# Kernel tuning notes

Hardware: AMD Instinct MI355X
Metric: run time of the kernel (lower is better)

The kernel has to match this reference:

```python
import jax, jax.numpy as jnp
import numpy as np
import math

T, NE, DA = 4096, 2048, 2048
LAYER_ID, NUM_LAYERS = 12, 24


def setup_inputs() -> dict:
    key = jax.random.key(0)
    kx, kk, kv, kr, ko = jax.random.split(key, 5)
    # --- learned params, initialised exactly like the haiku module ---
    ratio_0_to_1 = LAYER_ID / (NUM_LAYERS - 1)
    ratio_1_to_almost0 = 1.0 - LAYER_ID / NUM_LAYERS
    time_first = jnp.ones(DA, jnp.float32) * math.log(0.3) + \
        jnp.array([(i + 1) % 3 - 1 for i in range(DA)], jnp.float32) * 0.5
    time_decay = -5 + 8 * (jnp.arange(DA, dtype=jnp.float32) / (DA - 1)) ** (0.7 + 1.3 * ratio_0_to_1)
    ddd = jnp.arange(DA, dtype=jnp.float32)[jnp.newaxis, :] / DA  # [1, DA]
    time_mix_k = jnp.power(ddd, ratio_1_to_almost0)
    time_mix_v = time_mix_k + 0.3 * ratio_0_to_1
    time_mix_r = jnp.power(ddd, ratio_1_to_almost0 * 0.5)
    s = 1.0 / math.sqrt(NE)
    return {
        'x': jax.random.normal(kx, (T, NE), jnp.float32),
        'time_first': time_first,
        'time_decay': time_decay,
        'time_mix_k': time_mix_k,
        'time_mix_v': time_mix_v,
        'time_mix_r': time_mix_r,
        'W_key': jax.random.normal(kk, (NE, DA), jnp.float32) * s,
        'W_value': jax.random.normal(kv, (NE, DA), jnp.float32) * s,
        'W_receptance': jax.random.normal(kr, (NE, DA), jnp.float32) * s,
        'W_output': jax.random.normal(ko, (DA, NE), jnp.float32) * (1.0 / math.sqrt(DA)),
    }


def _wkv(time_decay, time_first, k, v):
    # k, v: [T, C]. Vectorized over channels; sequential scan over time.
    dtype = k.dtype
    w = -jnp.exp(time_decay.astype(jnp.float32))  # [C]
    u = time_first.astype(jnp.float32)            # [C]
    kf = k.astype(jnp.float32)
    vf = v.astype(jnp.float32)
    C = kf.shape[1]

    def body(carry, kv):
        p, q, o = carry
        kt, vt = kv
        # output at t (includes bonus u on current token)
        no = jnp.maximum(o, u + kt)
        A = jnp.exp(o - no)
        B = jnp.exp(u + kt - no)
        y = (A * p + B * vt) / (A * q + B)
        # state update (decay w applied to running sums)
        no2 = jnp.maximum(w + o, kt)
        A2 = jnp.exp(w + o - no2)
        B2 = jnp.exp(kt - no2)
        return (A2 * p + B2 * vt, A2 * q + B2, no2), y

    init = (jnp.zeros(C, jnp.float32), jnp.zeros(C, jnp.float32),
            jnp.full(C, -1e38, jnp.float32))
    _, ys = jax.lax.scan(body, init, (kf, vf))  # ys: [T, C]
    return ys.astype(dtype)


def reference(x, time_first, time_decay, time_mix_k, time_mix_v, time_mix_r,
              W_key, W_value, W_receptance, W_output):
    # time shift: shift sequence right by one (zero-pad first position)
    xx = jnp.pad(x, [(1, 0), (0, 0)])[:-1, :]
    xk = x * time_mix_k + xx * (1 - time_mix_k)
    xv = x * time_mix_v + xx * (1 - time_mix_v)
    xr = x * time_mix_r + xx * (1 - time_mix_r)
    k = xk @ W_key          # [T, DA]
    v = xv @ W_value        # [T, DA]
    r = xr @ W_receptance   # [T, DA]
    sr = jax.nn.sigmoid(r)
    wkv = _wkv(time_decay, time_first, k, v)  # [T, DA]
    return (sr * wkv) @ W_output              # [T, NE]
```

## Files before the change

kernel.cpp:

```cpp
#include <hip/hip_runtime.h>
#include <math.h>

#define T_ 4096
#define NE_ 2048
#define DA_ 2048
#define TDA ((size_t)T_ * NE_)

constexpr int NC = 64;
constexpr int CL = T_ / NC;

typedef __attribute__((ext_vector_type(8))) short short8;
typedef __attribute__((ext_vector_type(4))) float f32x4;

__device__ __forceinline__ unsigned short f2bf(float f) {
  union { float f; unsigned int u; } v; v.f = f;
  unsigned int u = v.u;
  return (unsigned short)((u + 0x7FFFu + ((u >> 16) & 1u)) >> 16);
}
__device__ __forceinline__ float bf2f(unsigned short h) {
  union { unsigned int u; float f; } v; v.u = ((unsigned int)h) << 16;
  return v.f;
}

__device__ __forceinline__ void gload_lds16(const void* g, void* l) {
  __builtin_amdgcn_global_load_lds(
      (const __attribute__((address_space(1))) void*)g,
      (__attribute__((address_space(3))) void*)l, 16, 0, 0);
}

__device__ __forceinline__ void gemm_core(
    const unsigned short* __restrict__ A, const unsigned short* __restrict__ Bt,
    void* __restrict__ C, int c_bf16)
{
  constexpr int K = 2048, N = 2048;
  __shared__ unsigned short As[128 * 32];
  __shared__ unsigned short Bs[128 * 32];

  const int tid = threadIdx.x;
  const int w = tid >> 6, lane = tid & 63;
  const int bm = blockIdx.x * 128, bn = blockIdx.y * 128;
  const int wr = w >> 1, wc = w & 1;

  f32x4 acc[4][4];
#pragma unroll
  for (int m = 0; m < 4; ++m)
#pragma unroll
    for (int n = 0; n < 4; ++n) acc[m][n] = (f32x4){0.f, 0.f, 0.f, 0.f};

  const int sr = lane >> 2;
  const int gc = (lane & 3) ^ ((lane >> 3) & 3);
  const size_t gA0 = (size_t)(bm + w * 32 + sr) * K + gc * 8;
  const size_t gB0 = (size_t)(bn + w * 32 + sr) * K + gc * 8;
  unsigned short* lA = &As[w * 1024];
  unsigned short* lB = &Bs[w * 1024];

  const int lr = lane & 15, ck = lane >> 4;
  const int coff = ((ck ^ ((lr >> 1) & 3)) << 3);
  const int arow = wr * 64 + lr;
  const int brow = wc * 64 + lr;

  for (int kk = 0; kk < K; kk += 32) {
    __syncthreads();
    gload_lds16(A + gA0 + kk, lA);
    gload_lds16(A + gA0 + kk + (size_t)16 * K, lA + 512);
    gload_lds16(Bt + gB0 + kk, lB);
    gload_lds16(Bt + gB0 + kk + (size_t)16 * K, lB + 512);
    __syncthreads();

    short8 af[4], bfr[4];
#pragma unroll
    for (int m = 0; m < 4; ++m)
      af[m] = *reinterpret_cast<const short8*>(&As[(arow + m * 16) * 32 + coff]);
#pragma unroll
    for (int n = 0; n < 4; ++n)
      bfr[n] = *reinterpret_cast<const short8*>(&Bs[(brow + n * 16) * 32 + coff]);
#pragma unroll
    for (int m = 0; m < 4; ++m)
#pragma unroll
      for (int n = 0; n < 4; ++n)
        acc[m][n] = __builtin_amdgcn_mfma_f32_16x16x32_bf16(af[m], bfr[n], acc[m][n], 0, 0, 0);
  }

  const int crow0 = bm + wr * 64 + (lane >> 4) * 4;
  const int ccol0 = bn + wc * 64 + (lane & 15);
  if (c_bf16) {
    unsigned short* Cb = (unsigned short*)C;
#pragma unroll
    for (int m = 0; m < 4; ++m)
#pragma unroll
      for (int n = 0; n < 4; ++n)
#pragma unroll
        for (int j = 0; j < 4; ++j)
          Cb[(size_t)(crow0 + m * 16 + j) * N + ccol0 + n * 16] = f2bf(acc[m][n][j]);
  } else {
    float* Cf = (float*)C;
#pragma unroll
    for (int m = 0; m < 4; ++m)
#pragma unroll
      for (int n = 0; n < 4; ++n)
#pragma unroll
        for (int j = 0; j < 4; ++j)
          Cf[(size_t)(crow0 + m * 16 + j) * N + ccol0 + n * 16] = acc[m][n][j];
  }
}

__global__ __launch_bounds__(256) void gemm3_bf16(
    const unsigned short* __restrict__ A0, const unsigned short* __restrict__ A1,
    const unsigned short* __restrict__ A2,
    const unsigned short* __restrict__ B0, const unsigned short* __restrict__ B1,
    const unsigned short* __restrict__ B2,
    void* __restrict__ C0, void* __restrict__ C1, void* __restrict__ C2,
    int c_bf16)
{
  const int z = blockIdx.z;
  const unsigned short* A = (z == 0) ? A0 : (z == 1) ? A1 : A2;
  const unsigned short* B = (z == 0) ? B0 : (z == 1) ? B1 : B2;
  void* C = (z == 0) ? C0 : (z == 1) ? C1 : C2;
  gemm_core(A, B, C, c_bf16);
}

__global__ __launch_bounds__(256) void transpose_cvt3(
    const float* __restrict__ W0, const float* __restrict__ W1,
    const float* __restrict__ W2,
    unsigned short* __restrict__ O0, unsigned short* __restrict__ O1,
    unsigned short* __restrict__ O2)
{
  constexpr int K = 2048, N = 2048;
  const int z = blockIdx.z;
  const float* W = (z == 0) ? W0 : (z == 1) ? W1 : W2;
  unsigned short* O = (z == 0) ? O0 : (z == 1) ? O1 : O2;

  __shared__ float tile[32][33];
  const int bk = blockIdx.y * 32;
  const int bn = blockIdx.x * 32;
  const int tx = threadIdx.x;
  const int ty = threadIdx.y;
#pragma unroll
  for (int i = 0; i < 32; i += 8)
    tile[ty + i][tx] = W[(size_t)(bk + ty + i) * N + bn + tx];
  __syncthreads();
#pragma unroll
  for (int i = 0; i < 32; i += 8)
    O[(size_t)(bn + ty + i) * K + bk + tx] = f2bf(tile[tx][ty + i]);
}

__global__ __launch_bounds__(256) void mix3_cvt(
    const float* __restrict__ x,
    const float* __restrict__ tmk, const float* __restrict__ tmv,
    const float* __restrict__ tmr,
    unsigned short* __restrict__ ok, unsigned short* __restrict__ ov,
    unsigned short* __restrict__ orr)
{
  const int i = blockIdx.x * 256 + threadIdx.x;
  const int t = i / (NE_ / 4);
  const int e4 = i % (NE_ / 4);
  const float4 xc = reinterpret_cast<const float4*>(x)[i];
  float4 xp = make_float4(0.f, 0.f, 0.f, 0.f);
  if (t > 0) xp = reinterpret_cast<const float4*>(x)[i - NE_ / 4];
  const float4 dx = make_float4(xc.x - xp.x, xc.y - xp.y, xc.z - xp.z, xc.w - xp.w);

  float4 m;
  ushort4 r;
  m = reinterpret_cast<const float4*>(tmk)[e4];
  r.x = f2bf(xp.x + m.x * dx.x); r.y = f2bf(xp.y + m.y * dx.y);
  r.z = f2bf(xp.z + m.z * dx.z); r.w = f2bf(xp.w + m.w * dx.w);
  reinterpret_cast<ushort4*>(ok)[i] = r;
  m = reinterpret_cast<const float4*>(tmv)[e4];
  r.x = f2bf(xp.x + m.x * dx.x); r.y = f2bf(xp.y + m.y * dx.y);
  r.z = f2bf(xp.z + m.z * dx.z); r.w = f2bf(xp.w + m.w * dx.w);
  reinterpret_cast<ushort4*>(ov)[i] = r;
  m = reinterpret_cast<const float4*>(tmr)[e4];
  r.x = f2bf(xp.x + m.x * dx.x); r.y = f2bf(xp.y + m.y * dx.y);
  r.z = f2bf(xp.z + m.z * dx.z); r.w = f2bf(xp.w + m.w * dx.w);
  reinterpret_cast<ushort4*>(orr)[i] = r;
}

__global__ __launch_bounds__(256) void wkv_pass1(
    const unsigned short* __restrict__ Kb, const unsigned short* __restrict__ Vb,
    const float* __restrict__ td, float* __restrict__ SP, float* __restrict__ SQ)
{
  const int c4 = blockIdx.x * 256 + threadIdx.x;
  const int chunk = blockIdx.y;
  const int t0 = chunk * CL;
  const float4 tdv = reinterpret_cast<const float4*>(td)[c4];
  float lam[4] = {__expf(-__expf(tdv.x)), __expf(-__expf(tdv.y)),
                  __expf(-__expf(tdv.z)), __expf(-__expf(tdv.w))};
  float P[4] = {0.f, 0.f, 0.f, 0.f}, Q[4] = {0.f, 0.f, 0.f, 0.f};
  for (int t = t0; t < t0 + CL; ++t) {
    const ushort4 kq = reinterpret_cast<const ushort4*>(Kb + (size_t)t * DA_)[c4];
    const ushort4 vq = reinterpret_cast<const ushort4*>(Vb + (size_t)t * DA_)[c4];
    const float kf[4] = {bf2f(kq.x), bf2f(kq.y), bf2f(kq.z), bf2f(kq.w)};
    const float vf[4] = {bf2f(vq.x), bf2f(vq.y), bf2f(vq.z), bf2f(vq.w)};
#pragma unroll
    for (int j = 0; j < 4; ++j) {
      const float e = __expf(kf[j]);
      P[j] = fmaf(lam[j], P[j], e * vf[j]);
      Q[j] = fmaf(lam[j], Q[j], e);
    }
  }
  reinterpret_cast<float4*>(SP + (size_t)chunk * DA_)[c4] = (float4){P[0], P[1], P[2], P[3]};
  reinterpret_cast<float4*>(SQ + (size_t)chunk * DA_)[c4] = (float4){Q[0], Q[1], Q[2], Q[3]};
}

__global__ __launch_bounds__(256) void wkv_pass2(
    const float* __restrict__ td, float* __restrict__ SP, float* __restrict__ SQ)
{
  const int c4 = blockIdx.x * 256 + threadIdx.x;
  const float4 tdv = reinterpret_cast<const float4*>(td)[c4];
  float lamL[4] = {__expf(-__expf(tdv.x) * (float)CL), __expf(-__expf(tdv.y) * (float)CL),
                   __expf(-__expf(tdv.z) * (float)CL), __expf(-__expf(tdv.w) * (float)CL)};
  float P[4] = {0.f, 0.f, 0.f, 0.f}, Q[4] = {0.f, 0.f, 0.f, 0.f};
  for (int i = 0; i < NC; ++i) {
    float4* sp4 = reinterpret_cast<float4*>(SP + (size_t)i * DA_) + c4;
    float4* sq4 = reinterpret_cast<float4*>(SQ + (size_t)i * DA_) + c4;
    const float4 sp = *sp4, sq = *sq4;
    *sp4 = (float4){P[0], P[1], P[2], P[3]};
    *sq4 = (float4){Q[0], Q[1], Q[2], Q[3]};
    P[0] = fmaf(lamL[0], P[0], sp.x); Q[0] = fmaf(lamL[0], Q[0], sq.x);
    P[1] = fmaf(lamL[1], P[1], sp.y); Q[1] = fmaf(lamL[1], Q[1], sq.y);
    P[2] = fmaf(lamL[2], P[2], sp.z); Q[2] = fmaf(lamL[2], Q[2], sq.z);
    P[3] = fmaf(lamL[3], P[3], sp.w); Q[3] = fmaf(lamL[3], Q[3], sq.w);
  }
}

__global__ __launch_bounds__(256) void wkv_pass3(
    const unsigned short* __restrict__ Kb, const unsigned short* __restrict__ Vb,
    const unsigned short* __restrict__ Rb, unsigned short* __restrict__ Ab,
    const float* __restrict__ td, const float* __restrict__ tf,
    const float* __restrict__ SP, const float* __restrict__ SQ)
{
  const int c4 = blockIdx.x * 256 + threadIdx.x;
  const int chunk = blockIdx.y;
  const int t0 = chunk * CL;
  const float4 tdv = reinterpret_cast<const float4*>(td)[c4];
  const float4 tfv = reinterpret_cast<const float4*>(tf)[c4];
  const float lam[4] = {__expf(-__expf(tdv.x)), __expf(-__expf(tdv.y)),
                        __expf(-__expf(tdv.z)), __expf(-__expf(tdv.w))};
  const float eu[4] = {__expf(tfv.x), __expf(tfv.y), __expf(tfv.z), __expf(tfv.w)};
  const float4 p0 = reinterpret_cast<const float4*>(SP + (size_t)chunk * DA_)[c4];
  const float4 q0 = reinterpret_cast<const float4*>(SQ + (size_t)chunk * DA_)[c4];
  float P[4] = {p0.x, p0.y, p0.z, p0.w};
  float Q[4] = {q0.x, q0.y, q0.z, q0.w};
  for (int t = t0; t < t0 + CL; ++t) {
    const ushort4 kq = reinterpret_cast<const ushort4*>(Kb + (size_t)t * DA_)[c4];
    const ushort4 vq = reinterpret_cast<const ushort4*>(Vb + (size_t)t * DA_)[c4];
    const ushort4 rq = reinterpret_cast<const ushort4*>(Rb + (size_t)t * DA_)[c4];
    const float kf[4] = {bf2f(kq.x), bf2f(kq.y), bf2f(kq.z), bf2f(kq.w)};
    const float vf[4] = {bf2f(vq.x), bf2f(vq.y), bf2f(vq.z), bf2f(vq.w)};
    const float rf[4] = {bf2f(rq.x), bf2f(rq.y), bf2f(rq.z), bf2f(rq.w)};
    ushort4 a;
    unsigned short* ap = (unsigned short*)&a;
#pragma unroll
    for (int j = 0; j < 4; ++j) {
      const float e = __expf(kf[j]);
      const float b = eu[j] * e;
      const float y = (P[j] + b * vf[j]) / (Q[j] + b);
      const float sr = 1.f / (1.f + __expf(-rf[j]));
      ap[j] = f2bf(sr * y);
      P[j] = fmaf(lam[j], P[j], e * vf[j]);
      Q[j] = fmaf(lam[j], Q[j], e);
    }
    reinterpret_cast<ushort4*>(Ab + (size_t)t * DA_)[c4] = a;
  }
}

extern "C" void kernel_launch(void* const* d_in, const int* in_sizes, int n_in,
                              void* d_out, int out_size, void* d_ws, size_t ws_size,
                              hipStream_t stream)
{
  const float* x   = (const float*)d_in[0];
  const float* tf  = (const float*)d_in[1];
  const float* td  = (const float*)d_in[2];
  const float* tmk = (const float*)d_in[3];
  const float* tmv = (const float*)d_in[4];
  const float* tmr = (const float*)d_in[5];
  const float* Wk  = (const float*)d_in[6];
  const float* Wv  = (const float*)d_in[7];
  const float* Wr  = (const float*)d_in[8];
  const float* Wo  = (const float*)d_in[9];
  float* out = (float*)d_out;

  const size_t MB = 1024 * 1024;
  char* ws = (char*)d_ws;

  const dim3 blk(256);
  const dim3 tblk(32, 8);
  const dim3 ggrid1(T_ / 128, DA_ / 128, 1);
  const size_t NEED_BATCH = 122 * MB;

  if (ws_size >= NEED_BATCH) {
    unsigned short* xmk = (unsigned short*)(ws + 0 * MB);
    unsigned short* xmv = (unsigned short*)(ws + 16 * MB);
    unsigned short* xmr = (unsigned short*)(ws + 32 * MB);
    unsigned short* WtK = (unsigned short*)(ws + 48 * MB);
    unsigned short* WtV = (unsigned short*)(ws + 56 * MB);
    unsigned short* WtR = (unsigned short*)(ws + 64 * MB);
    unsigned short* kb  = (unsigned short*)(ws + 72 * MB);
    unsigned short* vb  = (unsigned short*)(ws + 88 * MB);
    unsigned short* rb  = (unsigned short*)(ws + 104 * MB);
    float* sp = (float*)(ws + 120 * MB);
    float* sq = (float*)(ws + 120 * MB + 512 * 1024);

    transpose_cvt3<<<dim3(64, 64, 3), tblk, 0, stream>>>(Wk, Wv, Wr, WtK, WtV, WtR);
    mix3_cvt<<<TDA / 4 / 256, blk, 0, stream>>>(x, tmk, tmv, tmr, xmk, xmv, xmr);
    gemm3_bf16<<<dim3(T_ / 128, DA_ / 128, 3), blk, 0, stream>>>(
        xmk, xmv, xmr, WtK, WtV, WtR, kb, vb, rb, 1);

    wkv_pass1<<<dim3(DA_ / 4 / 256, NC), blk, 0, stream>>>(kb, vb, td, sp, sq);
    wkv_pass2<<<dim3(DA_ / 4 / 256), blk, 0, stream>>>(td, sp, sq);
    wkv_pass3<<<dim3(DA_ / 4 / 256, NC), blk, 0, stream>>>(kb, vb, rb, xmk, td, tf, sp, sq);

    transpose_cvt3<<<dim3(64, 64, 1), tblk, 0, stream>>>(Wo, Wo, Wo, WtK, WtK, WtK);
    gemm3_bf16<<<ggrid1, blk, 0, stream>>>(xmk, xmk, xmk, WtK, WtK, WtK, out, out, out, 0);
  } else {
    unsigned short* xmk = (unsigned short*)(ws + 0 * MB);
    unsigned short* xmv = (unsigned short*)(ws + 16 * MB);
    unsigned short* xmr = (unsigned short*)(ws + 32 * MB);
    unsigned short* Wt  = (unsigned short*)(ws + 48 * MB);
    unsigned short* kb  = (unsigned short*)(ws + 56 * MB);
    unsigned short* vb  = (unsigned short*)(ws + 72 * MB);
    unsigned short* rb  = (unsigned short*)(ws + 88 * MB);
    float* sp = (float*)(ws + 104 * MB);
    float* sq = (float*)(ws + 104 * MB + 512 * 1024);

    mix3_cvt<<<TDA / 4 / 256, blk, 0, stream>>>(x, tmk, tmv, tmr, xmk, xmv, xmr);
    transpose_cvt3<<<dim3(64, 64, 1), tblk, 0, stream>>>(Wk, Wk, Wk, Wt, Wt, Wt);
    gemm3_bf16<<<ggrid1, blk, 0, stream>>>(xmk, xmk, xmk, Wt, Wt, Wt, kb, kb, kb, 1);
    transpose_cvt3<<<dim3(64, 64, 1), tblk, 0, stream>>>(Wv, Wv, Wv, Wt, Wt, Wt);
    gemm3_bf16<<<ggrid1, blk, 0, stream>>>(xmv, xmv, xmv, Wt, Wt, Wt, vb, vb, vb, 1);
    transpose_cvt3<<<dim3(64, 64, 1), tblk, 0, stream>>>(Wr, Wr, Wr, Wt, Wt, Wt);
    gemm3_bf16<<<ggrid1, blk, 0, stream>>>(xmr, xmr, xmr, Wt, Wt, Wt, rb, rb, rb, 1);

    wkv_pass1<<<dim3(DA_ / 4 / 256, NC), blk, 0, stream>>>(kb, vb, td, sp, sq);
    wkv_pass2<<<dim3(DA_ / 4 / 256), blk, 0, stream>>>(td, sp, sq);
    wkv_pass3<<<dim3(DA_ / 4 / 256, NC), blk, 0, stream>>>(kb, vb, rb, xmk, td, tf, sp, sq);

    transpose_cvt3<<<dim3(64, 64, 1), tblk, 0, stream>>>(Wo, Wo, Wo, Wt, Wt, Wt);
    gemm3_bf16<<<ggrid1, blk, 0, stream>>>(xmk, xmk, xmk, Wt, Wt, Wt, out, out, out, 0);
  }
}
```

Baseline: 421.1 us.

## Double GEMM K-tile, widen WKV chunk parallelism, scalarize prefix pass

The GEMM core now stages a 64-wide K slice per iteration with an XOR swizzle over 8 column groups, which halves the number of barrier pairs per K loop at the cost of twice the LDS per block. The WKV scan doubles the number of time chunks and shrinks its blocks to 64 threads, putting many more workgroups on the GPU for the latency-bound sequential loops, and adds unroll hints. The chunk-prefix pass becomes per-channel scalar with batched loads of 16 chunks to expose memory parallelism. The SP/SQ buffers are spaced a full MB apart to fit the larger chunk count, and the Wo transpose is issued before the WKV passes.

```diff
diff --git a/kernel.cpp b/kernel.cpp
--- a/kernel.cpp
+++ b/kernel.cpp
@@ -6,7 +6,7 @@
 #define DA_ 2048
 #define TDA ((size_t)T_ * NE_)
 
-constexpr int NC = 64;
+constexpr int NC = 128;
 constexpr int CL = T_ / NC;
 
 typedef __attribute__((ext_vector_type(8))) short short8;
@@ -33,8 +33,8 @@
     void* __restrict__ C, int c_bf16)
 {
   constexpr int K = 2048, N = 2048;
-  __shared__ unsigned short As[128 * 32];
-  __shared__ unsigned short Bs[128 * 32];
+  __shared__ unsigned short As[128 * 64];
+  __shared__ unsigned short Bs[128 * 64];
 
   const int tid = threadIdx.x;
   const int w = tid >> 6, lane = tid & 63;
@@ -47,38 +47,43 @@
 #pragma unroll
     for (int n = 0; n < 4; ++n) acc[m][n] = (f32x4){0.f, 0.f, 0.f, 0.f};
 
-  const int sr = lane >> 2;
-  const int gc = (lane & 3) ^ ((lane >> 3) & 3);
-  const size_t gA0 = (size_t)(bm + w * 32 + sr) * K + gc * 8;
-  const size_t gB0 = (size_t)(bn + w * 32 + sr) * K + gc * 8;
-  unsigned short* lA = &As[w * 1024];
-  unsigned short* lB = &Bs[w * 1024];
+  const int sr8 = lane >> 3;
+  const int gcs = (lane & 7) ^ sr8;
+  const size_t gA0 = (size_t)(bm + w * 32 + sr8) * K + gcs * 8;
+  const size_t gB0 = (size_t)(bn + w * 32 + sr8) * K + gcs * 8;
+  unsigned short* lA = &As[(w * 32) * 64];
+  unsigned short* lB = &Bs[(w * 32) * 64];
 
   const int lr = lane & 15, ck = lane >> 4;
-  const int coff = ((ck ^ ((lr >> 1) & 3)) << 3);
+  const int x7 = lr & 7;
   const int arow = wr * 64 + lr;
   const int brow = wc * 64 + lr;
 
-  for (int kk = 0; kk < K; kk += 32) {
+  for (int kk = 0; kk < K; kk += 64) {
     __syncthreads();
-    gload_lds16(A + gA0 + kk, lA);
-    gload_lds16(A + gA0 + kk + (size_t)16 * K, lA + 512);
-    gload_lds16(Bt + gB0 + kk, lB);
-    gload_lds16(Bt + gB0 + kk + (size_t)16 * K, lB + 512);
+#pragma unroll
+    for (int g = 0; g < 4; ++g) {
+      gload_lds16(A + gA0 + kk + (size_t)(g * 8) * K, lA + g * 512);
+      gload_lds16(Bt + gB0 + kk + (size_t)(g * 8) * K, lB + g * 512);
+    }
     __syncthreads();
 
-    short8 af[4], bfr[4];
-#pragma unroll
-    for (int m = 0; m < 4; ++m)
-      af[m] = *reinterpret_cast<const short8*>(&As[(arow + m * 16) * 32 + coff]);
-#pragma unroll
-    for (int n = 0; n < 4; ++n)
-      bfr[n] = *reinterpret_cast<const short8*>(&Bs[(brow + n * 16) * 32 + coff]);
-#pragma unroll
-    for (int m = 0; m < 4; ++m)
+#pragma unroll
+    for (int s = 0; s < 2; ++s) {
+      const int c0 = ((s * 4 + ck) ^ x7) * 8;
+      short8 af[4], bfr[4];
+#pragma unroll
+      for (int m = 0; m < 4; ++m)
+        af[m] = *reinterpret_cast<const short8*>(&As[(arow + m * 16) * 64 + c0]);
 #pragma unroll
       for (int n = 0; n < 4; ++n)
-        acc[m][n] = __builtin_amdgcn_mfma_f32_16x16x32_bf16(af[m], bfr[n], acc[m][n], 0, 0, 0);
+        bfr[n] = *reinterpret_cast<const short8*>(&Bs[(brow + n * 16) * 64 + c0]);
+#pragma unroll
+      for (int m = 0; m < 4; ++m)
+#pragma unroll
+        for (int n = 0; n < 4; ++n)
+          acc[m][n] = __builtin_amdgcn_mfma_f32_16x16x32_bf16(af[m], bfr[n], acc[m][n], 0, 0, 0);
+    }
   }
 
   const int crow0 = bm + wr * 64 + (lane >> 4) * 4;
@@ -175,17 +180,18 @@
   reinterpret_cast<ushort4*>(orr)[i] = r;
 }
 
-__global__ __launch_bounds__(256) void wkv_pass1(
+__global__ __launch_bounds__(64) void wkv_pass1(
     const unsigned short* __restrict__ Kb, const unsigned short* __restrict__ Vb,
     const float* __restrict__ td, float* __restrict__ SP, float* __restrict__ SQ)
 {
-  const int c4 = blockIdx.x * 256 + threadIdx.x;
+  const int c4 = blockIdx.x * 64 + threadIdx.x;
   const int chunk = blockIdx.y;
   const int t0 = chunk * CL;
   const float4 tdv = reinterpret_cast<const float4*>(td)[c4];
   float lam[4] = {__expf(-__expf(tdv.x)), __expf(-__expf(tdv.y)),
                   __expf(-__expf(tdv.z)), __expf(-__expf(tdv.w))};
   float P[4] = {0.f, 0.f, 0.f, 0.f}, Q[4] = {0.f, 0.f, 0.f, 0.f};
+#pragma unroll 4
   for (int t = t0; t < t0 + CL; ++t) {
     const ushort4 kq = reinterpret_cast<const ushort4*>(Kb + (size_t)t * DA_)[c4];
     const ushort4 vq = reinterpret_cast<const ushort4*>(Vb + (size_t)t * DA_)[c4];
@@ -205,31 +211,33 @@
 __global__ __launch_bounds__(256) void wkv_pass2(
     const float* __restrict__ td, float* __restrict__ SP, float* __restrict__ SQ)
 {
-  const int c4 = blockIdx.x * 256 + threadIdx.x;
-  const float4 tdv = reinterpret_cast<const float4*>(td)[c4];
-  float lamL[4] = {__expf(-__expf(tdv.x) * (float)CL), __expf(-__expf(tdv.y) * (float)CL),
-                   __expf(-__expf(tdv.z) * (float)CL), __expf(-__expf(tdv.w) * (float)CL)};
-  float P[4] = {0.f, 0.f, 0.f, 0.f}, Q[4] = {0.f, 0.f, 0.f, 0.f};
-  for (int i = 0; i < NC; ++i) {
-    float4* sp4 = reinterpret_cast<float4*>(SP + (size_t)i * DA_) + c4;
-    float4* sq4 = reinterpret_cast<float4*>(SQ + (size_t)i * DA_) + c4;
-    const float4 sp = *sp4, sq = *sq4;
-    *sp4 = (float4){P[0], P[1], P[2], P[3]};
-    *sq4 = (float4){Q[0], Q[1], Q[2], Q[3]};
-    P[0] = fmaf(lamL[0], P[0], sp.x); Q[0] = fmaf(lamL[0], Q[0], sq.x);
-    P[1] = fmaf(lamL[1], P[1], sp.y); Q[1] = fmaf(lamL[1], Q[1], sq.y);
-    P[2] = fmaf(lamL[2], P[2], sp.z); Q[2] = fmaf(lamL[2], Q[2], sq.z);
-    P[3] = fmaf(lamL[3], P[3], sp.w); Q[3] = fmaf(lamL[3], Q[3], sq.w);
-  }
-}
-
-__global__ __launch_bounds__(256) void wkv_pass3(
+  const int c = blockIdx.x * 256 + threadIdx.x;
+  const float lamL = __expf(-__expf(td[c]) * (float)CL);
+  float P = 0.f, Q = 0.f;
+  for (int i0 = 0; i0 < NC; i0 += 16) {
+    float sp[16], sq[16];
+#pragma unroll
+    for (int j = 0; j < 16; ++j) {
+      sp[j] = SP[(size_t)(i0 + j) * DA_ + c];
+      sq[j] = SQ[(size_t)(i0 + j) * DA_ + c];
+    }
+#pragma unroll
+    for (int j = 0; j < 16; ++j) {
+      SP[(size_t)(i0 + j) * DA_ + c] = P;
+      SQ[(size_t)(i0 + j) * DA_ + c] = Q;
+      P = fmaf(lamL, P, sp[j]);
+      Q = fmaf(lamL, Q, sq[j]);
+    }
+  }
+}
+
+__global__ __launch_bounds__(64) void wkv_pass3(
     const unsigned short* __restrict__ Kb, const unsigned short* __restrict__ Vb,
     const unsigned short* __restrict__ Rb, unsigned short* __restrict__ Ab,
     const float* __restrict__ td, const float* __restrict__ tf,
     const float* __restrict__ SP, const float* __restrict__ SQ)
 {
-  const int c4 = blockIdx.x * 256 + threadIdx.x;
+  const int c4 = blockIdx.x * 64 + threadIdx.x;
   const int chunk = blockIdx.y;
   const int t0 = chunk * CL;
   const float4 tdv = reinterpret_cast<const float4*>(td)[c4];
@@ -241,6 +249,7 @@
   const float4 q0 = reinterpret_cast<const float4*>(SQ + (size_t)chunk * DA_)[c4];
   float P[4] = {p0.x, p0.y, p0.z, p0.w};
   float Q[4] = {q0.x, q0.y, q0.z, q0.w};
+#pragma unroll 4
   for (int t = t0; t < t0 + CL; ++t) {
     const ushort4 kq = reinterpret_cast<const ushort4*>(Kb + (size_t)t * DA_)[c4];
     const ushort4 vq = reinterpret_cast<const ushort4*>(Vb + (size_t)t * DA_)[c4];
@@ -284,8 +293,10 @@
   char* ws = (char*)d_ws;
 
   const dim3 blk(256);
+  const dim3 wblk(64);
   const dim3 tblk(32, 8);
   const dim3 ggrid1(T_ / 128, DA_ / 128, 1);
+  const dim3 wgrid(DA_ / 4 / 64, NC);
   const size_t NEED_BATCH = 122 * MB;
 
   if (ws_size >= NEED_BATCH) {
@@ -299,18 +310,19 @@
     unsigned short* vb  = (unsigned short*)(ws + 88 * MB);
     unsigned short* rb  = (unsigned short*)(ws + 104 * MB);
     float* sp = (float*)(ws + 120 * MB);
-    float* sq = (float*)(ws + 120 * MB + 512 * 1024);
+    float* sq = (float*)(ws + 121 * MB);
 
     transpose_cvt3<<<dim3(64, 64, 3), tblk, 0, stream>>>(Wk, Wv, Wr, WtK, WtV, WtR);
     mix3_cvt<<<TDA / 4 / 256, blk, 0, stream>>>(x, tmk, tmv, tmr, xmk, xmv, xmr);
     gemm3_bf16<<<dim3(T_ / 128, DA_ / 128, 3), blk, 0, stream>>>(
         xmk, xmv, xmr, WtK, WtV, WtR, kb, vb, rb, 1);
 
-    wkv_pass1<<<dim3(DA_ / 4 / 256, NC), blk, 0, stream>>>(kb, vb, td, sp, sq);
-    wkv_pass2<<<dim3(DA_ / 4 / 256), blk, 0, stream>>>(td, sp, sq);
-    wkv_pass3<<<dim3(DA_ / 4 / 256, NC), blk, 0, stream>>>(kb, vb, rb, xmk, td, tf, sp, sq);
-
     transpose_cvt3<<<dim3(64, 64, 1), tblk, 0, stream>>>(Wo, Wo, Wo, WtK, WtK, WtK);
+
+    wkv_pass1<<<wgrid, wblk, 0, stream>>>(kb, vb, td, sp, sq);
+    wkv_pass2<<<dim3(DA_ / 256), blk, 0, stream>>>(td, sp, sq);
+    wkv_pass3<<<wgrid, wblk, 0, stream>>>(kb, vb, rb, xmk, td, tf, sp, sq);
+
     gemm3_bf16<<<ggrid1, blk, 0, stream>>>(xmk, xmk, xmk, WtK, WtK, WtK, out, out, out, 0);
   } else {
     unsigned short* xmk = (unsigned short*)(ws + 0 * MB);
@@ -321,7 +333,7 @@
     unsigned short* vb  = (unsigned short*)(ws + 72 * MB);
     unsigned short* rb  = (unsigned short*)(ws + 88 * MB);
     float* sp = (float*)(ws + 104 * MB);
-    float* sq = (float*)(ws + 104 * MB + 512 * 1024);
+    float* sq = (float*)(ws + 105 * MB);
 
     mix3_cvt<<<TDA / 4 / 256, blk, 0, stream>>>(x, tmk, tmv, tmr, xmk, xmv, xmr);
     transpose_cvt3<<<dim3(64, 64, 1), tblk, 0, stream>>>(Wk, Wk, Wk, Wt, Wt, Wt);
@@ -331,9 +343,9 @@
     transpose_cvt3<<<dim3(64, 64, 1), tblk, 0, stream>>>(Wr, Wr, Wr, Wt, Wt, Wt);
     gemm3_bf16<<<ggrid1, blk, 0, stream>>>(xmr, xmr, xmr, Wt, Wt, Wt, rb, rb, rb, 1);
 
-    wkv_pass1<<<dim3(DA_ / 4 / 256, NC), blk, 0, stream>>>(kb, vb, td, sp, sq);
-    wkv_pass2<<<dim3(DA_ / 4 / 256), blk, 0, stream>>>(td, sp, sq);
-    wkv_pass3<<<dim3(DA_ / 4 / 256, NC), blk, 0, stream>>>(kb, vb, rb, xmk, td, tf, sp, sq);
+    wkv_pass1<<<wgrid, wblk, 0, stream>>>(kb, vb, td, sp, sq);
+    wkv_pass2<<<dim3(DA_ / 256), blk, 0, stream>>>(td, sp, sq);
+    wkv_pass3<<<wgrid, wblk, 0, stream>>>(kb, vb, rb, xmk, td, tf, sp, sq);
 
     transpose_cvt3<<<dim3(64, 64, 1), tblk, 0, stream>>>(Wo, Wo, Wo, Wt, Wt, Wt);
     gemm3_bf16<<<ggrid1, blk, 0, stream>>>(xmk, xmk, xmk, Wt, Wt, Wt, out, out, out, 0);
```

New measurement: 350.0 us. 1.2x faster.
